# Kernel tuning notes

Hardware: AMD Instinct MI355X
Metric: run time of the kernel (lower is better)

The kernel has to match this reference:

```python
import jax, jax.numpy as jnp
import numpy as np

N_M, N_D, E, D, H, O = 50000, 20000, 600000, 128, 128, 64


def _graph_conv(x_src, x_dst, src, dst, W_rel, b_rel, W_root, ew=None):
    # PyG GraphConv: lin_rel(scatter_add(msg)) + lin_root(x_dst)
    msg = x_src[src]                       # [E, d_src] gather
    if ew is not None:
        msg = msg * ew[:, None]            # edge-weighted messages
    agg = jax.ops.segment_sum(msg, dst, num_segments=x_dst.shape[0])  # [N_dst, d_src]
    return agg @ W_rel + b_rel + x_dst @ W_root


def setup_inputs() -> dict:
    key = jax.random.key(0)
    ks = jax.random.split(key, 16)
    s = 1.0 / np.sqrt(D)
    inp = {
        "x_meas": jax.random.normal(ks[0], (N_M, D), jnp.float32),
        "x_dem": jax.random.normal(ks[1], (N_D, D), jnp.float32),
        "src_m": jax.random.randint(ks[2], (E,), 0, N_M, jnp.int32),
        "dst_m": jax.random.randint(ks[3], (E,), 0, N_M, jnp.int32),
        "src_b": jax.random.randint(ks[4], (E,), 0, N_M, jnp.int32),
        "dst_b": jax.random.randint(ks[5], (E,), 0, N_D, jnp.int32),
        "edge_weight": jax.random.normal(ks[6], (E,), jnp.float32),
        "W_rel1": jax.random.normal(ks[7], (D, H), jnp.float32) * s,
        "b_rel1": jnp.zeros((H,), jnp.float32),
        "W_root1": jax.random.normal(ks[8], (D, H), jnp.float32) * s,
        "W_rel2": jax.random.normal(ks[9], (D, H), jnp.float32) * s,
        "b_rel2": jnp.zeros((H,), jnp.float32),
        "W_root2": jax.random.normal(ks[10], (D, H), jnp.float32) * s,
        "W_rel3": jax.random.normal(ks[11], (H, H), jnp.float32) * s,
        "b_rel3": jnp.zeros((H,), jnp.float32),
        "W_root3": jax.random.normal(ks[12], (H, H), jnp.float32) * s,
        "W_lin": jax.random.normal(ks[13], (H, O), jnp.float32) * (1.0 / np.sqrt(H)),
        "b_lin": jnp.zeros((O,), jnp.float32),
    }
    return inp


def reference(x_meas, x_dem, src_m, dst_m, src_b, dst_b, edge_weight,
              W_rel1, b_rel1, W_root1, W_rel2, b_rel2, W_root2,
              W_rel3, b_rel3, W_root3, W_lin, b_lin):
    ew = jax.nn.sigmoid(edge_weight)
    movie_x = jax.nn.relu(_graph_conv(x_meas, x_meas, src_m, dst_m, W_rel1, b_rel1, W_root1))
    user_x = jax.nn.relu(_graph_conv(x_meas, x_dem, src_b, dst_b, W_rel2, b_rel2, W_root2, ew))
    user_x = jax.nn.relu(_graph_conv(movie_x, user_x, src_b, dst_b, W_rel3, b_rel3, W_root3, ew))
    return user_x @ W_lin + b_lin  # [N_D, O]
```

## Files before the change

### kernel.cpp

```cpp
#include <hip/hip_runtime.h>


typedef unsigned short u16;
typedef unsigned int u32;
typedef __attribute__((ext_vector_type(8))) short bf16x8;
typedef __attribute__((ext_vector_type(4))) float f32x4;

__device__ __forceinline__ float bf2f(u16 h) {
    union { u32 u; float f; } v; v.u = ((u32)h) << 16; return v.f;
}
__device__ __forceinline__ u16 f2bf(float f) {
    union { float f; u32 u; } v; v.f = f;
    u32 lsb = (v.u >> 16) & 1u;
    v.u += 0x7fffu + lsb;
    return (u16)(v.u >> 16);
}

__global__ __launch_bounds__(256)
void prep_kernel(const int* __restrict__ dst_m, const int* __restrict__ dst_b,
                 int* __restrict__ deg_m, int* __restrict__ deg_b,
                 int* __restrict__ rank_m, int* __restrict__ rank_b, int E,
                 const float* __restrict__ xm, u16* __restrict__ xm_bf, int n8m,
                 const float* __restrict__ xd, u16* __restrict__ xd_bf, int n8d,
                 const float* __restrict__ w0, const float* __restrict__ w1,
                 const float* __restrict__ w2, const float* __restrict__ w3,
                 const float* __restrict__ w4, const float* __restrict__ w5,
                 const float* __restrict__ w6, u16* __restrict__ wbuf,
                 int HB, int TB, int TB2)
{
    const int b = blockIdx.x;
    if (b < HB) {
        int t = b * 256 + threadIdx.x;
        if (t < E) {
            rank_m[t] = atomicAdd(&deg_m[dst_m[t]], 1);
        } else if (t < 2 * E) {
            int e = t - E;
            rank_b[e] = atomicAdd(&deg_b[dst_b[e]], 1);
        }
    } else if (b < HB + TB + TB2) {
        const bool isM = b < HB + TB;
        const float* src = isM ? xm : xd;
        u16* dst = isM ? xm_bf : xd_bf;
        int n8 = isM ? n8m : n8d;
        int i = (b - (isM ? HB : HB + TB)) * 256 + threadIdx.x;
        if (i >= n8) return;
        float4 a = ((const float4*)src)[2 * i];
        float4 c = ((const float4*)src)[2 * i + 1];
        ushort4 h0; h0.x = f2bf(a.x); h0.y = f2bf(a.y); h0.z = f2bf(a.z); h0.w = f2bf(a.w);
        ushort4 h1; h1.x = f2bf(c.x); h1.y = f2bf(c.y); h1.z = f2bf(c.z); h1.w = f2bf(c.w);
        ((ushort4*)dst)[2 * i]     = h0;
        ((ushort4*)dst)[2 * i + 1] = h1;
    } else {
        int bb = b - HB - TB - TB2;
        const int widx = bb >> 6;
        const int o    = ((bb & 63) << 8) + threadIdx.x;
        const int OC   = (widx == 6) ? 64 : 128;
        if (o >= OC * 128) return;
        const float* W;
        switch (widx) {
            case 0: W = w0; break; case 1: W = w1; break; case 2: W = w2; break;
            case 3: W = w3; break; case 4: W = w4; break; case 5: W = w5; break;
            default: W = w6;
        }
        int j = o & 7;
        int lane = (o >> 3) & 63;
        int n, c;
        if (OC == 128) { n = (o >> 9) & 7; c = o >> 12; }
        else           { n = (o >> 9) & 3; c = o >> 11; }
        int col = n * 16 + (lane & 15);
        int k   = c * 32 + (lane >> 4) * 8 + j;
        wbuf[widx * 16384 + o] = f2bf(W[k * OC + col]);
    }
}

__device__ __forceinline__ int wave_incl_scan(int v, int lane) {
#pragma unroll
    for (int off = 1; off < 64; off <<= 1) {
        int t = __shfl_up(v, off, 64);
        if (lane >= off) v += t;
    }
    return v;
}

__global__ __launch_bounds__(1024)
void scan2_kernel(const int* __restrict__ degA, int* __restrict__ rpA, int nA,
                  const int* __restrict__ degB, int* __restrict__ rpB, int nB)
{
    const int* deg = blockIdx.x ? degB : degA;
    int* rp = blockIdx.x ? rpB : rpA;
    int n = blockIdx.x ? nB : nA;

    __shared__ int wsum[16];
    __shared__ int carry;
    const int tid = threadIdx.x, lane = tid & 63, wid = tid >> 6;
    if (tid == 0) carry = 0;
    __syncthreads();

    for (int base = 0; base < n; base += 4096) {
        int idx = base + tid * 4;
        int4 v = make_int4(0, 0, 0, 0);
        if (idx + 3 < n) v = *(const int4*)(deg + idx);
        else {
            if (idx + 0 < n) v.x = deg[idx + 0];
            if (idx + 1 < n) v.y = deg[idx + 1];
            if (idx + 2 < n) v.z = deg[idx + 2];
            if (idx + 3 < n) v.w = deg[idx + 3];
        }
        int s = v.x + v.y + v.z + v.w;
        int incl = wave_incl_scan(s, lane);
        if (lane == 63) wsum[wid] = incl;
        __syncthreads();
        if (wid == 0) {
            int t = (lane < 16) ? wsum[lane] : 0;
            int ti = wave_incl_scan(t, lane);
            if (lane < 16) wsum[lane] = ti - t;
        }
        __syncthreads();
        int base_t = carry + wsum[wid] + incl - s;
        if (idx + 3 < n) {
            int4 st;
            st.x = base_t;
            st.y = base_t + v.x;
            st.z = base_t + v.x + v.y;
            st.w = base_t + v.x + v.y + v.z;
            *(int4*)(rp + idx) = st;
        } else {
            if (idx + 0 < n) rp[idx + 0] = base_t;
            if (idx + 1 < n) rp[idx + 1] = base_t + v.x;
            if (idx + 2 < n) rp[idx + 2] = base_t + v.x + v.y;
            if (idx + 3 < n) rp[idx + 3] = base_t + v.x + v.y + v.z;
        }
        __syncthreads();
        if (tid == 1023) carry += wsum[15] + incl;
        __syncthreads();
    }
    if (tid == 0) rp[n] = carry;
}

__global__ __launch_bounds__(256)
void fill_kernel(const int* __restrict__ src_m, const int* __restrict__ dst_m,
                 const int* __restrict__ src_b, const int* __restrict__ dst_b,
                 const float* __restrict__ edge_w,
                 const int* __restrict__ rp_m, const int* __restrict__ rp_b,
                 const int* __restrict__ rank_m, const int* __restrict__ rank_b,
                 int* __restrict__ srcs_m, int2* __restrict__ edges_b, int E)
{
    int t = blockIdx.x * 256 + threadIdx.x;
    if (t < E) {
        int pos = rp_m[dst_m[t]] + rank_m[t];
        srcs_m[pos] = src_m[t];
    } else if (t < 2 * E) {
        int e = t - E;
        int pos = rp_b[dst_b[e]] + rank_b[e];
        float x = edge_w[e];
        int2 pk;
        pk.x = src_b[e];
        pk.y = __float_as_int(1.0f / (1.0f + __expf(-x)));
        edges_b[pos] = pk;
    }
}

__global__ __launch_bounds__(256)
void gather12(const u16* __restrict__ Xb,
              const int* __restrict__ srcs_m, const int2* __restrict__ edges_b,
              const int* __restrict__ rp_m, const int* __restrict__ rp_b,
              u16* __restrict__ agg1, u16* __restrict__ agg2, int NM, int ND)
{
    const int h  = blockIdx.x * 8 + (threadIdx.x >> 5);
    const int cl = threadIdx.x & 31;
    float4 acc = make_float4(0.f, 0.f, 0.f, 0.f);

    if (h < NM) {
        int i   = rp_m[h];
        int end = rp_m[h + 1];
        for (; i + 4 <= end; i += 4) {
            int s0 = srcs_m[i], s1 = srcs_m[i + 1], s2 = srcs_m[i + 2], s3 = srcs_m[i + 3];
            ushort4 v0 = *(const ushort4*)(Xb + (size_t)s0 * 128 + cl * 4);
            ushort4 v1 = *(const ushort4*)(Xb + (size_t)s1 * 128 + cl * 4);
            ushort4 v2 = *(const ushort4*)(Xb + (size_t)s2 * 128 + cl * 4);
            ushort4 v3 = *(const ushort4*)(Xb + (size_t)s3 * 128 + cl * 4);
            acc.x += (bf2f(v0.x) + bf2f(v1.x)) + (bf2f(v2.x) + bf2f(v3.x));
            acc.y += (bf2f(v0.y) + bf2f(v1.y)) + (bf2f(v2.y) + bf2f(v3.y));
            acc.z += (bf2f(v0.z) + bf2f(v1.z)) + (bf2f(v2.z) + bf2f(v3.z));
            acc.w += (bf2f(v0.w) + bf2f(v1.w)) + (bf2f(v2.w) + bf2f(v3.w));
        }
        for (; i < end; ++i) {
            int s = srcs_m[i];
            ushort4 v = *(const ushort4*)(Xb + (size_t)s * 128 + cl * 4);
            acc.x += bf2f(v.x); acc.y += bf2f(v.y);
            acc.z += bf2f(v.z); acc.w += bf2f(v.w);
        }
        ushort4 st;
        st.x = f2bf(acc.x); st.y = f2bf(acc.y);
        st.z = f2bf(acc.z); st.w = f2bf(acc.w);
        *(ushort4*)(agg1 + (size_t)h * 128 + cl * 4) = st;
    } else if (h < NM + ND) {
        int node = h - NM;
        int i   = rp_b[node];
        int end = rp_b[node + 1];
        for (; i + 4 <= end; i += 4) {
            int2 p0 = edges_b[i],     p1 = edges_b[i + 1];
            int2 p2 = edges_b[i + 2], p3 = edges_b[i + 3];
            float w0 = __int_as_float(p0.y), w1 = __int_as_float(p1.y);
            float w2 = __int_as_float(p2.y), w3 = __int_as_float(p3.y);
            ushort4 v0 = *(const ushort4*)(Xb + (size_t)p0.x * 128 + cl * 4);
            ushort4 v1 = *(const ushort4*)(Xb + (size_t)p1.x * 128 + cl * 4);
            ushort4 v2 = *(const ushort4*)(Xb + (size_t)p2.x * 128 + cl * 4);
            ushort4 v3 = *(const ushort4*)(Xb + (size_t)p3.x * 128 + cl * 4);
            acc.x = fmaf(w0, bf2f(v0.x), acc.x); acc.y = fmaf(w0, bf2f(v0.y), acc.y);
            acc.z = fmaf(w0, bf2f(v0.z), acc.z); acc.w = fmaf(w0, bf2f(v0.w), acc.w);
            acc.x = fmaf(w1, bf2f(v1.x), acc.x); acc.y = fmaf(w1, bf2f(v1.y), acc.y);
            acc.z = fmaf(w1, bf2f(v1.z), acc.z); acc.w = fmaf(w1, bf2f(v1.w), acc.w);
            acc.x = fmaf(w2, bf2f(v2.x), acc.x); acc.y = fmaf(w2, bf2f(v2.y), acc.y);
            acc.z = fmaf(w2, bf2f(v2.z), acc.z); acc.w = fmaf(w2, bf2f(v2.w), acc.w);
            acc.x = fmaf(w3, bf2f(v3.x), acc.x); acc.y = fmaf(w3, bf2f(v3.y), acc.y);
            acc.z = fmaf(w3, bf2f(v3.z), acc.z); acc.w = fmaf(w3, bf2f(v3.w), acc.w);
        }
        for (; i < end; ++i) {
            int2 pk = edges_b[i];
            float w = __int_as_float(pk.y);
            ushort4 v = *(const ushort4*)(Xb + (size_t)pk.x * 128 + cl * 4);
            acc.x = fmaf(w, bf2f(v.x), acc.x); acc.y = fmaf(w, bf2f(v.y), acc.y);
            acc.z = fmaf(w, bf2f(v.z), acc.z); acc.w = fmaf(w, bf2f(v.w), acc.w);
        }
        ushort4 st;
        st.x = f2bf(acc.x); st.y = f2bf(acc.y);
        st.z = f2bf(acc.z); st.w = f2bf(acc.w);
        *(ushort4*)(agg2 + (size_t)node * 128 + cl * 4) = st;
    }
}

__global__ __launch_bounds__(256)
void gather3_kernel(const u16* __restrict__ Mv, const int2* __restrict__ edges_b,
                    const int* __restrict__ rp_b, u16* __restrict__ agg3, int ND)
{
    const int node = blockIdx.x * 8 + (threadIdx.x >> 5);
    if (node >= ND) return;
    const int cl = threadIdx.x & 31;
    int i   = rp_b[node];
    int end = rp_b[node + 1];

    float4 acc = make_float4(0.f, 0.f, 0.f, 0.f);
    for (; i + 4 <= end; i += 4) {
        int2 p0 = edges_b[i],     p1 = edges_b[i + 1];
        int2 p2 = edges_b[i + 2], p3 = edges_b[i + 3];
        float w0 = __int_as_float(p0.y), w1 = __int_as_float(p1.y);
        float w2 = __int_as_float(p2.y), w3 = __int_as_float(p3.y);
        ushort4 v0 = *(const ushort4*)(Mv + (size_t)p0.x * 128 + cl * 4);
        ushort4 v1 = *(const ushort4*)(Mv + (size_t)p1.x * 128 + cl * 4);
        ushort4 v2 = *(const ushort4*)(Mv + (size_t)p2.x * 128 + cl * 4);
        ushort4 v3 = *(const ushort4*)(Mv + (size_t)p3.x * 128 + cl * 4);
        acc.x = fmaf(w0, bf2f(v0.x), acc.x); acc.y = fmaf(w0, bf2f(v0.y), acc.y);
        acc.z = fmaf(w0, bf2f(v0.z), acc.z); acc.w = fmaf(w0, bf2f(v0.w), acc.w);
        acc.x = fmaf(w1, bf2f(v1.x), acc.x); acc.y = fmaf(w1, bf2f(v1.y), acc.y);
        acc.z = fmaf(w1, bf2f(v1.z), acc.z); acc.w = fmaf(w1, bf2f(v1.w), acc.w);
        acc.x = fmaf(w2, bf2f(v2.x), acc.x); acc.y = fmaf(w2, bf2f(v2.y), acc.y);
        acc.z = fmaf(w2, bf2f(v2.z), acc.z); acc.w = fmaf(w2, bf2f(v2.w), acc.w);
        acc.x = fmaf(w3, bf2f(v3.x), acc.x); acc.y = fmaf(w3, bf2f(v3.y), acc.y);
        acc.z = fmaf(w3, bf2f(v3.z), acc.z); acc.w = fmaf(w3, bf2f(v3.w), acc.w);
    }
    for (; i < end; ++i) {
        int2 pk = edges_b[i];
        float w = __int_as_float(pk.y);
        ushort4 v = *(const ushort4*)(Mv + (size_t)pk.x * 128 + cl * 4);
        acc.x = fmaf(w, bf2f(v.x), acc.x); acc.y = fmaf(w, bf2f(v.y), acc.y);
        acc.z = fmaf(w, bf2f(v.z), acc.z); acc.w = fmaf(w, bf2f(v.w), acc.w);
    }
    ushort4 st;
    st.x = f2bf(acc.x); st.y = f2bf(acc.y);
    st.z = f2bf(acc.z); st.w = f2bf(acc.w);
    *(ushort4*)(agg3 + (size_t)node * 128 + cl * 4) = st;
}

__global__ __launch_bounds__(256)
void conv12_mfma(const u16* __restrict__ agg1, const u16* __restrict__ w1r,
                 const float* __restrict__ b1, const u16* __restrict__ xm_bf,
                 const u16* __restrict__ w1o, u16* __restrict__ C1, int N1, int cb1,
                 const u16* __restrict__ agg2, const u16* __restrict__ w2r,
                 const float* __restrict__ b2, const u16* __restrict__ xd_bf,
                 const u16* __restrict__ w2o, u16* __restrict__ C2, int N2)
{
    __shared__ u16 sW[16384];

    const bool seg1 = (int)blockIdx.x < cb1;
    const u16 *A0, *A1p, *Wr, *Wo; const float* bias; u16* C; int N, base;
    if (seg1) { A0 = agg1; A1p = xm_bf; Wr = w1r; Wo = w1o; bias = b1; C = C1; N = N1; base = blockIdx.x; }
    else      { A0 = agg2; A1p = xd_bf; Wr = w2r; Wo = w2o; bias = b2; C = C2; N = N2; base = blockIdx.x - cb1; }

    const int tid  = threadIdx.x;
    const int lane = tid & 63;
    const int m0   = (base * 4 + (tid >> 6)) * 32;
    const int lr   = lane & 15;
    const int quad = lane >> 4;

    int r0 = m0 + lr;      if (r0 >= N) r0 = N - 1;
    int r1 = m0 + 16 + lr; if (r1 >= N) r1 = N - 1;

    f32x4 acc[2][8];
#pragma unroll
    for (int mt = 0; mt < 2; ++mt)
#pragma unroll
        for (int n = 0; n < 8; ++n) acc[mt][n] = (f32x4){0.f, 0.f, 0.f, 0.f};

    for (int i = tid; i < 2048; i += 256)
        ((uint4*)sW)[i] = ((const uint4*)Wr)[i];
    __syncthreads();
#pragma unroll
    for (int c = 0; c < 4; ++c) {
        const int kb = c * 32 + quad * 8;
        bf16x8 a0 = *(const bf16x8*)(A0 + (size_t)r0 * 128 + kb);
        bf16x8 a1 = *(const bf16x8*)(A0 + (size_t)r1 * 128 + kb);
        const u16* wp = sW + c * 4096 + lane * 8;
#pragma unroll
        for (int n = 0; n < 8; ++n) {
            bf16x8 b = *(const bf16x8*)(wp + n * 512);
            acc[0][n] = __builtin_amdgcn_mfma_f32_16x16x32_bf16(a0, b, acc[0][n], 0, 0, 0);
            acc[1][n] = __builtin_amdgcn_mfma_f32_16x16x32_bf16(a1, b, acc[1][n], 0, 0, 0);
        }
    }
    __syncthreads();

    for (int i = tid; i < 2048; i += 256)
        ((uint4*)sW)[i] = ((const uint4*)Wo)[i];
    __syncthreads();
#pragma unroll
    for (int c = 0; c < 4; ++c) {
        const int kb = c * 32 + quad * 8;
        bf16x8 a0 = *(const bf16x8*)(A1p + (size_t)r0 * 128 + kb);
        bf16x8 a1 = *(const bf16x8*)(A1p + (size_t)r1 * 128 + kb);
        const u16* wp = sW + c * 4096 + lane * 8;
#pragma unroll
        for (int n = 0; n < 8; ++n) {
            bf16x8 b = *(const bf16x8*)(wp + n * 512);
            acc[0][n] = __builtin_amdgcn_mfma_f32_16x16x32_bf16(a0, b, acc[0][n], 0, 0, 0);
            acc[1][n] = __builtin_amdgcn_mfma_f32_16x16x32_bf16(a1, b, acc[1][n], 0, 0, 0);
        }
    }

#pragma unroll
    for (int mt = 0; mt < 2; ++mt) {
#pragma unroll
        for (int n = 0; n < 8; ++n) {
            const int col = n * 16 + lr;
            const float b = bias[col];
#pragma unroll
            for (int r = 0; r < 4; ++r) {
                int row = m0 + mt * 16 + quad * 4 + r;
                if (row >= N) continue;
                C[(size_t)row * 128 + col] = f2bf(fmaxf(acc[mt][n][r] + b, 0.f));
            }
        }
    }
}

__global__ __launch_bounds__(256)
void conv3_lin(const u16* __restrict__ A1, const u16* __restrict__ Wr,
               const float* __restrict__ bias3,
               const u16* __restrict__ A2, const u16* __restrict__ Wo,
               const u16* __restrict__ Wl, const float* __restrict__ bias_l,
               float* __restrict__ out, int N)
{
    __shared__ u16 lds[17408 + 8192];
    u16* tile = lds;
    u16* sWl  = lds + 17408;

    const int tid  = threadIdx.x;
    const int lane = tid & 63;
    const int wv   = tid >> 6;
    const int wbase = wv * 32;
    const int m0   = (blockIdx.x * 4 + wv) * 32;
    const int lr   = lane & 15;
    const int quad = lane >> 4;

    int r0 = m0 + lr;      if (r0 >= N) r0 = N - 1;
    int r1 = m0 + 16 + lr; if (r1 >= N) r1 = N - 1;

    f32x4 acc[2][8];
#pragma unroll
    for (int mt = 0; mt < 2; ++mt)
#pragma unroll
        for (int n = 0; n < 8; ++n) acc[mt][n] = (f32x4){0.f, 0.f, 0.f, 0.f};

    for (int i = tid; i < 1024; i += 256)
        ((uint4*)sWl)[i] = ((const uint4*)Wl)[i];
    for (int i = tid; i < 2048; i += 256)
        ((uint4*)lds)[i] = ((const uint4*)Wr)[i];
    __syncthreads();
#pragma unroll
    for (int c = 0; c < 4; ++c) {
        const int kb = c * 32 + quad * 8;
        bf16x8 a0 = *(const bf16x8*)(A1 + (size_t)r0 * 128 + kb);
        bf16x8 a1 = *(const bf16x8*)(A1 + (size_t)r1 * 128 + kb);
        const u16* wp = lds + c * 4096 + lane * 8;
#pragma unroll
        for (int n = 0; n < 8; ++n) {
            bf16x8 b = *(const bf16x8*)(wp + n * 512);
            acc[0][n] = __builtin_amdgcn_mfma_f32_16x16x32_bf16(a0, b, acc[0][n], 0, 0, 0);
            acc[1][n] = __builtin_amdgcn_mfma_f32_16x16x32_bf16(a1, b, acc[1][n], 0, 0, 0);
        }
    }
    __syncthreads();
    for (int i = tid; i < 2048; i += 256)
        ((uint4*)lds)[i] = ((const uint4*)Wo)[i];
    __syncthreads();
#pragma unroll
    for (int c = 0; c < 4; ++c) {
        const int kb = c * 32 + quad * 8;
        bf16x8 a0 = *(const bf16x8*)(A2 + (size_t)r0 * 128 + kb);
        bf16x8 a1 = *(const bf16x8*)(A2 + (size_t)r1 * 128 + kb);
        const u16* wp = lds + c * 4096 + lane * 8;
#pragma unroll
        for (int n = 0; n < 8; ++n) {
            bf16x8 b = *(const bf16x8*)(wp + n * 512);
            acc[0][n] = __builtin_amdgcn_mfma_f32_16x16x32_bf16(a0, b, acc[0][n], 0, 0, 0);
            acc[1][n] = __builtin_amdgcn_mfma_f32_16x16x32_bf16(a1, b, acc[1][n], 0, 0, 0);
        }
    }
    __syncthreads();

#pragma unroll
    for (int mt = 0; mt < 2; ++mt) {
#pragma unroll
        for (int n = 0; n < 8; ++n) {
            const int col = n * 16 + lr;
            const float b = bias3[col];
#pragma unroll
            for (int r = 0; r < 4; ++r) {
                int row = wbase + mt * 16 + quad * 4 + r;
                tile[row * 136 + col] = f2bf(fmaxf(acc[mt][n][r] + b, 0.f));
            }
        }
    }
    __syncthreads();

    f32x4 acc2[2][4];
#pragma unroll
    for (int mt = 0; mt < 2; ++mt)
#pragma unroll
        for (int n = 0; n < 4; ++n) acc2[mt][n] = (f32x4){0.f, 0.f, 0.f, 0.f};

#pragma unroll
    for (int c = 0; c < 4; ++c) {
        const int kb = c * 32 + quad * 8;
        bf16x8 a0 = *(const bf16x8*)(tile + (wbase + lr) * 136 + kb);
        bf16x8 a1 = *(const bf16x8*)(tile + (wbase + 16 + lr) * 136 + kb);
#pragma unroll
        for (int n = 0; n < 4; ++n) {
            bf16x8 b = *(const bf16x8*)(sWl + c * 2048 + n * 512 + lane * 8);
            acc2[0][n] = __builtin_amdgcn_mfma_f32_16x16x32_bf16(a0, b, acc2[0][n], 0, 0, 0);
            acc2[1][n] = __builtin_amdgcn_mfma_f32_16x16x32_bf16(a1, b, acc2[1][n], 0, 0, 0);
        }
    }

#pragma unroll
    for (int mt = 0; mt < 2; ++mt) {
#pragma unroll
        for (int n = 0; n < 4; ++n) {
            const int col = n * 16 + lr;
            const float b = bias_l[col];
#pragma unroll
            for (int r = 0; r < 4; ++r) {
                int row = m0 + mt * 16 + quad * 4 + r;
                if (row >= N) continue;
                out[(size_t)row * 64 + col] = acc2[mt][n][r] + b;
            }
        }
    }
}

extern "C" void kernel_launch(void* const* d_in, const int* in_sizes, int n_in,
                              void* d_out, int out_size, void* d_ws, size_t ws_size,
                              hipStream_t stream)
{
    const float* x_meas  = (const float*)d_in[0];
    const float* x_dem   = (const float*)d_in[1];
    const int*   src_m   = (const int*)d_in[2];
    const int*   dst_m   = (const int*)d_in[3];
    const int*   src_b   = (const int*)d_in[4];
    const int*   dst_b   = (const int*)d_in[5];
    const float* edge_w  = (const float*)d_in[6];
    const float* W_rel1  = (const float*)d_in[7];
    const float* b_rel1  = (const float*)d_in[8];
    const float* W_root1 = (const float*)d_in[9];
    const float* W_rel2  = (const float*)d_in[10];
    const float* b_rel2  = (const float*)d_in[11];
    const float* W_root2 = (const float*)d_in[12];
    const float* W_rel3  = (const float*)d_in[13];
    const float* b_rel3  = (const float*)d_in[14];
    const float* W_root3 = (const float*)d_in[15];
    const float* W_lin   = (const float*)d_in[16];
    const float* b_lin   = (const float*)d_in[17];
    float* out = (float*)d_out;

    const int NM = 50000, ND = 20000, E = 600000;

    char* p = (char*)d_ws;
    auto alloc = [&](size_t bytes) { char* r = p; p += (bytes + 511) & ~(size_t)511; return r; };
    int*   deg_m   = (int*)alloc((size_t)NM * 4);
    int*   deg_b   = (int*)alloc((size_t)ND * 4);
    int*   rp_m    = (int*)alloc((size_t)(NM + 1) * 4);
    int*   rp_b    = (int*)alloc((size_t)(ND + 1) * 4);
    int*   srcs_m  = (int*)alloc((size_t)E * 4);
    int2*  edges_b = (int2*)alloc((size_t)E * 8);
    u16*   agg1    = (u16*)alloc((size_t)NM * 128 * 2);
    u16*   agg2    = (u16*)alloc((size_t)ND * 128 * 2);
    u16*   movie   = (u16*)alloc((size_t)NM * 128 * 2);
    u16*   t2      = (u16*)alloc((size_t)ND * 128 * 2);
    u16*   xd_bf   = (u16*)alloc((size_t)ND * 128 * 2);
    u16*   wbuf    = (u16*)alloc(7 * 16384 * 2);
    int* rank_m = (int*)agg1;
    int* rank_b = rank_m + E;
    u16* xm_bf  = movie;
    u16* agg3   = agg1;

    size_t deg_span = (size_t)((char*)deg_b - (char*)deg_m) + (size_t)ND * 4;
    hipMemsetAsync(deg_m, 0, deg_span, stream);

    const int HB  = (2 * E + 255) / 256;
    const int TB  = (NM * 16 + 255) / 256;
    const int TB2 = (ND * 16 + 255) / 256;
    const int WB  = 448;
    prep_kernel<<<HB + TB + TB2 + WB, 256, 0, stream>>>(
        dst_m, dst_b, deg_m, deg_b, rank_m, rank_b, E,
        x_meas, xm_bf, NM * 16, x_dem, xd_bf, ND * 16,
        W_rel1, W_root1, W_rel2, W_root2, W_rel3, W_root3, W_lin, wbuf,
        HB, TB, TB2);

    scan2_kernel<<<2, 1024, 0, stream>>>(deg_m, rp_m, NM, deg_b, rp_b, ND);
    fill_kernel<<<HB, 256, 0, stream>>>(src_m, dst_m, src_b, dst_b, edge_w,
                                        rp_m, rp_b, rank_m, rank_b, srcs_m, edges_b, E);

    gather12<<<(NM + ND + 7) / 8, 256, 0, stream>>>(xm_bf, srcs_m, edges_b,
                                                    rp_m, rp_b, agg1, agg2, NM, ND);

    const int cb1 = (NM + 127) / 128;
    const int cb2 = (ND + 127) / 128;
    u16* w1r = wbuf + 0 * 16384; u16* w1o = wbuf + 1 * 16384;
    u16* w2r = wbuf + 2 * 16384; u16* w2o = wbuf + 3 * 16384;
    u16* w3r = wbuf + 4 * 16384; u16* w3o = wbuf + 5 * 16384;
    u16* wl  = wbuf + 6 * 16384;
    conv12_mfma<<<cb1 + cb2, 256, 0, stream>>>(agg1, w1r, b_rel1, xm_bf, w1o, movie, NM, cb1,
                                               agg2, w2r, b_rel2, xd_bf, w2o, t2,    ND);

    gather3_kernel<<<(ND + 7) / 8, 256, 0, stream>>>(movie, edges_b, rp_b, agg3, ND);

    conv3_lin<<<cb2, 256, 0, stream>>>(agg3, w3r, b_rel3, t2, w3o, wl, b_lin, out, ND);
}
```

Measured before the change: 302.3 us.

## Replace global atomic degree histogram with per-chunk LDS histograms and column scan

```diff
diff --git a/kernel.cpp b/kernel.cpp
--- a/kernel.cpp
+++ b/kernel.cpp
@@ -5,6 +5,16 @@
 typedef unsigned int u32;
 typedef __attribute__((ext_vector_type(8))) short bf16x8;
 typedef __attribute__((ext_vector_type(4))) float f32x4;
+
+#define NMC 50000
+#define NDC 20000
+#define EC  600000
+#define CM  64
+#define CD  32
+#define CHM (EC / CM)
+#define CHD (EC / CD)
+#define NWM (NMC / 2)
+#define NWD (NDC / 2)
 
 __device__ __forceinline__ float bf2f(u16 h) {
     union { u32 u; float f; } v; v.u = ((u32)h) << 16; return v.f;
@@ -17,41 +27,69 @@
 }
 
 __global__ __launch_bounds__(256)
-void prep_kernel(const int* __restrict__ dst_m, const int* __restrict__ dst_b,
-                 int* __restrict__ deg_m, int* __restrict__ deg_b,
-                 int* __restrict__ rank_m, int* __restrict__ rank_b, int E,
-                 const float* __restrict__ xm, u16* __restrict__ xm_bf, int n8m,
-                 const float* __restrict__ xd, u16* __restrict__ xd_bf, int n8d,
-                 const float* __restrict__ w0, const float* __restrict__ w1,
-                 const float* __restrict__ w2, const float* __restrict__ w3,
-                 const float* __restrict__ w4, const float* __restrict__ w5,
-                 const float* __restrict__ w6, u16* __restrict__ wbuf,
-                 int HB, int TB, int TB2)
-{
+void hist_lds(const int* __restrict__ dst_m, const int* __restrict__ dst_b,
+              int* __restrict__ rank_m, int* __restrict__ rank_b,
+              u32* __restrict__ histm, u32* __restrict__ histd)
+{
+    __shared__ u32 h[NWM];
     const int b = blockIdx.x;
-    if (b < HB) {
-        int t = b * 256 + threadIdx.x;
-        if (t < E) {
-            rank_m[t] = atomicAdd(&deg_m[dst_m[t]], 1);
-        } else if (t < 2 * E) {
-            int e = t - E;
-            rank_b[e] = atomicAdd(&deg_b[dst_b[e]], 1);
-        }
-    } else if (b < HB + TB + TB2) {
-        const bool isM = b < HB + TB;
+    const bool isM = b < CM;
+    const int nw = isM ? NWM : NWD;
+    for (int i = threadIdx.x; i < nw; i += 256) h[i] = 0;
+    __syncthreads();
+    if (isM) {
+        const int e0 = b * CHM;
+        const int e1 = min(EC, e0 + CHM);
+        for (int e = e0 + threadIdx.x; e < e1; e += 256) {
+            int d = dst_m[e];
+            int sh = (d & 1) * 16;
+            u32 old = atomicAdd(&h[d >> 1], 1u << sh);
+            rank_m[e] = (old >> sh) & 0xffffu;
+        }
+        __syncthreads();
+        for (int i = threadIdx.x; i < nw; i += 256)
+            histm[(size_t)b * NWM + i] = h[i];
+    } else {
+        const int bb = b - CM;
+        const int e0 = bb * CHD;
+        const int e1 = min(EC, e0 + CHD);
+        for (int e = e0 + threadIdx.x; e < e1; e += 256) {
+            int d = dst_b[e];
+            int sh = (d & 1) * 16;
+            u32 old = atomicAdd(&h[d >> 1], 1u << sh);
+            rank_b[e] = (old >> sh) & 0xffffu;
+        }
+        __syncthreads();
+        for (int i = threadIdx.x; i < nw; i += 256)
+            histd[(size_t)bb * NWD + i] = h[i];
+    }
+}
+
+__global__ __launch_bounds__(256)
+void prep2(const float* __restrict__ xm, u16* __restrict__ xm_bf, int n8m,
+           const float* __restrict__ xd, u16* __restrict__ xd_bf, int n8d,
+           const float* __restrict__ w0, const float* __restrict__ w1,
+           const float* __restrict__ w2, const float* __restrict__ w3,
+           const float* __restrict__ w4, const float* __restrict__ w5,
+           const float* __restrict__ w6, u16* __restrict__ wbuf,
+           int TB, int TB2)
+{
+    const int b = blockIdx.x;
+    if (b < TB + TB2) {
+        const bool isM = b < TB;
         const float* src = isM ? xm : xd;
         u16* dst = isM ? xm_bf : xd_bf;
         int n8 = isM ? n8m : n8d;
-        int i = (b - (isM ? HB : HB + TB)) * 256 + threadIdx.x;
+        int i = (b - (isM ? 0 : TB)) * 256 + threadIdx.x;
         if (i >= n8) return;
         float4 a = ((const float4*)src)[2 * i];
-        float4 c = ((const float4*)src)[2 * i + 1];
+        float4 c2 = ((const float4*)src)[2 * i + 1];
         ushort4 h0; h0.x = f2bf(a.x); h0.y = f2bf(a.y); h0.z = f2bf(a.z); h0.w = f2bf(a.w);
-        ushort4 h1; h1.x = f2bf(c.x); h1.y = f2bf(c.y); h1.z = f2bf(c.z); h1.w = f2bf(c.w);
+        ushort4 h1; h1.x = f2bf(c2.x); h1.y = f2bf(c2.y); h1.z = f2bf(c2.z); h1.w = f2bf(c2.w);
         ((ushort4*)dst)[2 * i]     = h0;
         ((ushort4*)dst)[2 * i + 1] = h1;
     } else {
-        int bb = b - HB - TB - TB2;
+        int bb = b - TB - TB2;
         const int widx = bb >> 6;
         const int o    = ((bb & 63) << 8) + threadIdx.x;
         const int OC   = (widx == 6) ? 64 : 128;
@@ -71,6 +109,26 @@
         int k   = c * 32 + (lane >> 4) * 8 + j;
         wbuf[widx * 16384 + o] = f2bf(W[k * OC + col]);
     }
+}
+
+__global__ __launch_bounds__(256)
+void basescan2(u32* __restrict__ histm, u32* __restrict__ histd,
+               int* __restrict__ deg_m, int* __restrict__ deg_b)
+{
+    int w = blockIdx.x * 256 + threadIdx.x;
+    u32* hist; int* deg; int NW, C;
+    if (w < NWM)            { hist = histm; deg = deg_m; NW = NWM; C = CM; }
+    else if (w < NWM + NWD) { hist = histd; deg = deg_b; NW = NWD; C = CD; w -= NWM; }
+    else return;
+    u32 runlo = 0, runhi = 0;
+    for (int c = 0; c < C; ++c) {
+        u32 v = hist[(size_t)c * NW + w];
+        hist[(size_t)c * NW + w] = runlo | (runhi << 16);
+        runlo += v & 0xffffu;
+        runhi += v >> 16;
+    }
+    deg[2 * w]     = (int)runlo;
+    deg[2 * w + 1] = (int)runhi;
 }
 
 __device__ __forceinline__ int wave_incl_scan(int v, int lane) {
@@ -143,15 +201,24 @@
                  const float* __restrict__ edge_w,
                  const int* __restrict__ rp_m, const int* __restrict__ rp_b,
                  const int* __restrict__ rank_m, const int* __restrict__ rank_b,
+                 const u32* __restrict__ histm, const u32* __restrict__ histd,
                  int* __restrict__ srcs_m, int2* __restrict__ edges_b, int E)
 {
     int t = blockIdx.x * 256 + threadIdx.x;
     if (t < E) {
-        int pos = rp_m[dst_m[t]] + rank_m[t];
+        int d = dst_m[t];
+        int c = t / CHM;
+        u32 pk = histm[(size_t)c * NWM + (d >> 1)];
+        int base = (pk >> ((d & 1) * 16)) & 0xffffu;
+        int pos = rp_m[d] + base + rank_m[t];
         srcs_m[pos] = src_m[t];
     } else if (t < 2 * E) {
         int e = t - E;
-        int pos = rp_b[dst_b[e]] + rank_b[e];
+        int d = dst_b[e];
+        int c = e / CHD;
+        u32 pkb = histd[(size_t)c * NWD + (d >> 1)];
+        int base = (pkb >> ((d & 1) * 16)) & 0xffffu;
+        int pos = rp_b[d] + base + rank_b[e];
         float x = edge_w[e];
         int2 pk;
         pk.x = src_b[e];
@@ -492,10 +559,12 @@
     const float* b_lin   = (const float*)d_in[17];
     float* out = (float*)d_out;
 
-    const int NM = 50000, ND = 20000, E = 600000;
+    const int NM = NMC, ND = NDC, E = EC;
 
     char* p = (char*)d_ws;
     auto alloc = [&](size_t bytes) { char* r = p; p += (bytes + 511) & ~(size_t)511; return r; };
+    u32*   histm   = (u32*)alloc((size_t)CM * NWM * 4);
+    u32*   histd   = (u32*)alloc((size_t)CD * NWD * 4);
     int*   deg_m   = (int*)alloc((size_t)NM * 4);
     int*   deg_b   = (int*)alloc((size_t)ND * 4);
     int*   rp_m    = (int*)alloc((size_t)(NM + 1) * 4);
@@ -513,22 +582,23 @@
     u16* xm_bf  = movie;
     u16* agg3   = agg1;
 
-    size_t deg_span = (size_t)((char*)deg_b - (char*)deg_m) + (size_t)ND * 4;
-    hipMemsetAsync(deg_m, 0, deg_span, stream);
-
-    const int HB  = (2 * E + 255) / 256;
     const int TB  = (NM * 16 + 255) / 256;
     const int TB2 = (ND * 16 + 255) / 256;
     const int WB  = 448;
-    prep_kernel<<<HB + TB + TB2 + WB, 256, 0, stream>>>(
-        dst_m, dst_b, deg_m, deg_b, rank_m, rank_b, E,
+    const int HB  = (2 * E + 255) / 256;
+
+    hist_lds<<<CM + CD, 256, 0, stream>>>(dst_m, dst_b, rank_m, rank_b, histm, histd);
+
+    prep2<<<TB + TB2 + WB, 256, 0, stream>>>(
         x_meas, xm_bf, NM * 16, x_dem, xd_bf, ND * 16,
         W_rel1, W_root1, W_rel2, W_root2, W_rel3, W_root3, W_lin, wbuf,
-        HB, TB, TB2);
-
+        TB, TB2);
+
+    basescan2<<<(NWM + NWD + 255) / 256, 256, 0, stream>>>(histm, histd, deg_m, deg_b);
     scan2_kernel<<<2, 1024, 0, stream>>>(deg_m, rp_m, NM, deg_b, rp_b, ND);
     fill_kernel<<<HB, 256, 0, stream>>>(src_m, dst_m, src_b, dst_b, edge_w,
-                                        rp_m, rp_b, rank_m, rank_b, srcs_m, edges_b, E);
+                                        rp_m, rp_b, rank_m, rank_b,
+                                        histm, histd, srcs_m, edges_b, E);
 
     gather12<<<(NM + ND + 7) / 8, 256, 0, stream>>>(xm_bf, srcs_m, edges_b,
                                                     rp_m, rp_b, agg1, agg2, NM, ND);
```

After: 303.4 us. Within noise of the previous version (+0.4%).
